# Kernel tuning notes

Measured on AMD Instinct MI355X. Metric: run time of the kernel, lower is better.

Reference implementation:

```python
import jax, jax.numpy as jnp
import numpy as np

NEG = -9.0e15


def setup_inputs() -> dict:
    key = jax.random.key(0)
    ks = jax.random.split(key, 8)
    N, D_IN, D_OUT, EMB = 100000, 128, 128, 64
    E, NPE = 50000, 32   # hyperedges, nodes per edge
    U, EPN = 50000, 32   # output nodes, edges per node
    stdv = 1.0 / np.sqrt(D_IN)
    return {
        "x": jax.random.normal(ks[0], (N, D_IN), dtype=jnp.float32),
        "seq": jax.random.randint(ks[1], (E, NPE), 0, N, dtype=jnp.int64),
        "text2emb": jax.random.normal(ks[2], (100, EMB), dtype=jnp.float32),
        "useq": jax.random.randint(ks[3], (U, EPN), 0, E, dtype=jnp.int64),
        "data_idx": jax.random.randint(ks[4], (U,), 0, U, dtype=jnp.int64),
        "weight1": jax.random.uniform(ks[5], (D_IN, D_OUT), jnp.float32, -stdv, stdv),
        "weight2": jax.random.uniform(ks[6], (D_OUT, D_OUT), jnp.float32, -stdv, stdv),
        "weight3": jax.random.uniform(ks[7], (100, EMB), jnp.float32, -stdv, stdv),
    }


def _masked_mean_weights(idx):
    # softmax over a {1, -9e15} mask -> uniform weights over nonzero slots
    logits = jnp.where(idx > 0, jnp.float32(1.0), jnp.float32(NEG))
    return jax.nn.softmax(logits, axis=1)


def reference(x, seq, text2emb, useq, data_idx, weight1, weight2, weight3):
    # text_weight is computed in the original forward but never used
    w3n = weight3 / jnp.linalg.norm(weight3, axis=1, keepdims=True)
    cos = w3n @ w3n.T
    _text_weight = cos.mean(axis=1).mean()  # scalar, unused downstream

    h = x @ weight1                              # [N, D_OUT]
    adj_fea = h[seq]                             # [E, NPE, D_OUT] gather
    w = _masked_mean_weights(seq)                # [E, NPE]
    edge = jnp.einsum("enc,en->ec", adj_fea, w)  # [E, D_OUT]
    # dropout is identity in eval mode
    edge = jax.nn.relu(edge)
    e1 = edge @ weight2                          # [E, D_OUT]

    edge_fea = e1[useq]                          # [U, EPN, D_OUT] gather
    uw = _masked_mean_weights(useq)              # [U, EPN]
    node = jnp.einsum("uec,ue->uc", edge_fea, uw)  # [U, D_OUT]
    return node
```

## Files before the change

kernel.cpp:

```cpp
#include <hip/hip_runtime.h>
#include <hip/hip_bf16.h>

#define N_NODES  100000
#define E_EDGES  50000
#define U_NODES  50000
#define D        128
#define NPE      32

typedef __attribute__((ext_vector_type(8))) short short8;
typedef __attribute__((ext_vector_type(4))) unsigned short u16x4;
typedef __attribute__((ext_vector_type(4))) float f32x4;

static __device__ __forceinline__ unsigned short f2bf_bits(float f) {
    unsigned u = __float_as_uint(f);
    return (unsigned short)((u + 0x7fffu + ((u >> 16) & 1u)) >> 16);
}

__global__ void prep_wt(const float* __restrict__ w1, const float* __restrict__ w2,
                        unsigned short* __restrict__ wt) {
    const int t = blockIdx.x * 256 + threadIdx.x;
    const int which = t >> 14;
    const int e = t & 16383;
    const int k = e >> 7, c = e & 127;
    const float* w = which ? w2 : w1;
    wt[which * 16384 + c * 128 + k] = f2bf_bits(w[e]);
}

__global__ __launch_bounds__(256) void convert_x(const float* __restrict__ x,
                                                 unsigned short* __restrict__ xb,
                                                 int n8) {
    const int i = blockIdx.x * 256 + threadIdx.x;
    if (i >= n8) return;
    const float4 a = ((const float4*)x)[2 * i];
    const float4 b = ((const float4*)x)[2 * i + 1];
    uint4 o;
    o.x = (unsigned)f2bf_bits(a.x) | ((unsigned)f2bf_bits(a.y) << 16);
    o.y = (unsigned)f2bf_bits(a.z) | ((unsigned)f2bf_bits(a.w) << 16);
    o.z = (unsigned)f2bf_bits(b.x) | ((unsigned)f2bf_bits(b.y) << 16);
    o.w = (unsigned)f2bf_bits(b.z) | ((unsigned)f2bf_bits(b.w) << 16);
    ((uint4*)xb)[i] = o;
}

template<int OUT_BF16, int RELU>
__global__ __launch_bounds__(256) void gather_mean4(
        const unsigned short* __restrict__ src, const int* __restrict__ idx,
        void* __restrict__ dst, int M) {
    const int wid = (int)((blockIdx.x * blockDim.x + threadIdx.x) >> 6);
    if (wid >= M) return;
    const int lane = threadIdx.x & 63;
    const int g = lane >> 4;
    const int c = lane & 15;

    int my = 0;
    if (lane < NPE) my = idx[(size_t)wid * NPE + lane];
    const unsigned long long b = __ballot(lane < NPE && my > 0);
    const int count = __popcll(b);
    const float scale = 1.0f / (float)(count > 0 ? count : NPE);
    const bool take_all = (count == 0);

    uint4 v[8];
    float w[8];
#pragma unroll
    for (int i = 0; i < 8; ++i) {
        const int id = __shfl(my, i * 4 + g);
        w[i] = (take_all || id > 0) ? scale : 0.0f;
        v[i] = *(const uint4*)(src + (size_t)id * D + c * 8);
    }
    asm volatile("" ::: "memory");

    float acc[8] = {0.f, 0.f, 0.f, 0.f, 0.f, 0.f, 0.f, 0.f};
#pragma unroll
    for (int i = 0; i < 8; ++i) {
        acc[0] = fmaf(__uint_as_float(v[i].x << 16),         w[i], acc[0]);
        acc[1] = fmaf(__uint_as_float(v[i].x & 0xffff0000u), w[i], acc[1]);
        acc[2] = fmaf(__uint_as_float(v[i].y << 16),         w[i], acc[2]);
        acc[3] = fmaf(__uint_as_float(v[i].y & 0xffff0000u), w[i], acc[3]);
        acc[4] = fmaf(__uint_as_float(v[i].z << 16),         w[i], acc[4]);
        acc[5] = fmaf(__uint_as_float(v[i].z & 0xffff0000u), w[i], acc[5]);
        acc[6] = fmaf(__uint_as_float(v[i].w << 16),         w[i], acc[6]);
        acc[7] = fmaf(__uint_as_float(v[i].w & 0xffff0000u), w[i], acc[7]);
    }

#pragma unroll
    for (int i = 0; i < 8; ++i) {
        acc[i] += __shfl_xor(acc[i], 16);
        acc[i] += __shfl_xor(acc[i], 32);
        if (RELU) acc[i] = fmaxf(acc[i], 0.f);
    }

    if (lane < 16) {
        if (OUT_BF16) {
            uint4 o;
            o.x = (unsigned)f2bf_bits(acc[0]) | ((unsigned)f2bf_bits(acc[1]) << 16);
            o.y = (unsigned)f2bf_bits(acc[2]) | ((unsigned)f2bf_bits(acc[3]) << 16);
            o.z = (unsigned)f2bf_bits(acc[4]) | ((unsigned)f2bf_bits(acc[5]) << 16);
            o.w = (unsigned)f2bf_bits(acc[6]) | ((unsigned)f2bf_bits(acc[7]) << 16);
            *(uint4*)((unsigned short*)dst + (size_t)wid * D + c * 8) = o;
        } else {
            float* dp = (float*)dst + (size_t)wid * D + c * 8;
            *(float4*)dp = make_float4(acc[0], acc[1], acc[2], acc[3]);
            *(float4*)(dp + 4) = make_float4(acc[4], acc[5], acc[6], acc[7]);
        }
    }
}

__global__ __launch_bounds__(256) void gemm12(const unsigned short* __restrict__ gx,
                                              const unsigned short* __restrict__ Wt,
                                              unsigned short* __restrict__ e1, int M) {
    __shared__ unsigned short sW1[128 * 136];
    __shared__ unsigned short sW2[128 * 136];
    __shared__ unsigned short sA[64 * 136];
    const int tid = threadIdx.x;

    {
        const float4* w4 = (const float4*)Wt;
#pragma unroll
        for (int j = 0; j < 8; ++j) {
            const int i = tid + j * 256;
            const int r = i >> 4, c16 = i & 15;
            *(float4*)&sW1[r * 136 + c16 * 8] = w4[i];
            *(float4*)&sW2[r * 136 + c16 * 8] = w4[2048 + i];
        }
    }

    const int ntiles = (M + 63) >> 6;
    const int lane = tid & 63;
    const int wv = tid >> 6;
    const int r16 = lane & 15;
    const int hi = lane >> 4;

    float4 pf[4];
    auto load_tile = [&](int tile) {
        const int row0 = tile << 6;
#pragma unroll
        for (int j = 0; j < 4; ++j) {
            const int i = tid + j * 256;
            int gr = row0 + (i >> 4); if (gr >= M) gr = M - 1;
            pf[j] = *(const float4*)&gx[(size_t)gr * D + (i & 15) * 8];
        }
    };

    int tile = blockIdx.x;
    if (tile >= ntiles) return;
    load_tile(tile);

    while (tile < ntiles) {
#pragma unroll
        for (int j = 0; j < 4; ++j) {
            const int i = tid + j * 256;
            *(float4*)&sA[(i >> 4) * 136 + (i & 15) * 8] = pf[j];
        }
        __syncthreads();

        const int next = tile + gridDim.x;
        if (next < ntiles) load_tile(next);
        asm volatile("" ::: "memory");

        short8 af[4];
#pragma unroll
        for (int kt = 0; kt < 4; ++kt)
            af[kt] = *(const short8*)&sA[(wv * 16 + r16) * 136 + kt * 32 + hi * 8];

        f32x4 acc[8];
#pragma unroll
        for (int ct = 0; ct < 8; ++ct) acc[ct] = (f32x4){0.f, 0.f, 0.f, 0.f};
#pragma unroll
        for (int ct = 0; ct < 8; ++ct)
#pragma unroll
            for (int kt = 0; kt < 4; ++kt) {
                const short8 bf = *(const short8*)&sW1[(ct * 16 + r16) * 136 + kt * 32 + hi * 8];
                acc[ct] = __builtin_amdgcn_mfma_f32_16x16x32_bf16(af[kt], bf, acc[ct], 0, 0, 0);
            }

#pragma unroll
        for (int ct = 0; ct < 8; ++ct)
#pragma unroll
            for (int i = 0; i < 4; ++i)
                sA[(wv * 16 + hi * 4 + i) * 136 + ct * 16 + r16] =
                    f2bf_bits(fmaxf(acc[ct][i], 0.f));

        short8 af2[4];
#pragma unroll
        for (int kt = 0; kt < 4; ++kt)
            af2[kt] = *(const short8*)&sA[(wv * 16 + r16) * 136 + kt * 32 + hi * 8];

        f32x4 acc2[8];
#pragma unroll
        for (int ct = 0; ct < 8; ++ct) acc2[ct] = (f32x4){0.f, 0.f, 0.f, 0.f};
#pragma unroll
        for (int ct = 0; ct < 8; ++ct)
#pragma unroll
            for (int kt = 0; kt < 4; ++kt) {
                const short8 bf = *(const short8*)&sW2[(ct * 16 + r16) * 136 + kt * 32 + hi * 8];
                acc2[ct] = __builtin_amdgcn_mfma_f32_16x16x32_bf16(af2[kt], bf, acc2[ct], 0, 0, 0);
            }

#pragma unroll
        for (int ct = 0; ct < 8; ++ct)
#pragma unroll
            for (int i = 0; i < 4; ++i)
                sA[(wv * 16 + hi * 4 + i) * 136 + ct * 16 + r16] = f2bf_bits(acc2[ct][i]);
        __syncthreads();

        const int row0 = tile << 6;
        const int nrows = min(64, M - row0);
#pragma unroll
        for (int j = 0; j < 4; ++j) {
            const int i = tid + j * 256;
            const int r = i >> 4, cc = i & 15;
            if (r < nrows)
                *(float4*)&e1[(size_t)(row0 + r) * D + cc * 8] =
                    *(const float4*)&sA[r * 136 + cc * 8];
        }
        __syncthreads();
        tile = next;
    }
}

extern "C" void kernel_launch(void* const* d_in, const int* in_sizes, int n_in,
                              void* d_out, int out_size, void* d_ws, size_t ws_size,
                              hipStream_t stream) {
    const float* x    = (const float*)d_in[0];
    const int*   seq  = (const int*)d_in[1];
    const int*   useq = (const int*)d_in[3];
    const float* w1   = (const float*)d_in[5];
    const float* w2   = (const float*)d_in[6];
    float* out = (float*)d_out;

    unsigned short* wt = (unsigned short*)d_ws;
    unsigned short* xb = wt + 2 * 16384;
    unsigned short* gx = xb + (size_t)N_NODES * D;
    unsigned short* e1 = gx + (size_t)E_EDGES * D;

    prep_wt<<<128, 256, 0, stream>>>(w1, w2, wt);
    convert_x<<<(N_NODES * D / 8 + 255) / 256, 256, 0, stream>>>(x, xb, N_NODES * D / 8);

    gather_mean4<1, 0><<<(E_EDGES * 64) / 256, 256, 0, stream>>>(xb, seq, gx, E_EDGES);

    gemm12<<<512, 256, 0, stream>>>(gx, wt, e1, E_EDGES);

    gather_mean4<0, 0><<<(U_NODES * 64) / 256, 256, 0, stream>>>(e1, useq, out, U_NODES);
}
```

Measured before the change: 232.6 us.

## Restructure fused GEMM into one-shot 1024-thread tiles with XOR-swizzled LDS, inline-asm gather loads

The persistent 64-row tile loop in the fused two-GEMM kernel is replaced by one 256-row tile per 1024-thread block, with no cross-tile prefetch. LDS padding is replaced by an XOR swizzle to avoid bank conflicts. The gather kernel now issues its row loads through inline global_load_dwordx4 asm followed by an explicit waitcnt, so all eight loads stay in flight together. The larger blocks use about 128KB of LDS, which limits residency to one block per CU and drops overlap of loads with compute.

```diff
diff --git a/kernel.cpp b/kernel.cpp
--- a/kernel.cpp
+++ b/kernel.cpp
@@ -10,10 +10,15 @@
 typedef __attribute__((ext_vector_type(8))) short short8;
 typedef __attribute__((ext_vector_type(4))) unsigned short u16x4;
 typedef __attribute__((ext_vector_type(4))) float f32x4;
+typedef __attribute__((ext_vector_type(4))) unsigned int u32x4;
 
 static __device__ __forceinline__ unsigned short f2bf_bits(float f) {
     unsigned u = __float_as_uint(f);
     return (unsigned short)((u + 0x7fffu + ((u >> 16) & 1u)) >> 16);
+}
+
+static __device__ __forceinline__ int swz(int row, int bytecol) {
+    return row * 256 + ((((bytecol >> 4) ^ (row & 7)) << 4) | (bytecol & 15));
 }
 
 __global__ void prep_wt(const float* __restrict__ w1, const float* __restrict__ w2,
@@ -58,15 +63,19 @@
     const float scale = 1.0f / (float)(count > 0 ? count : NPE);
     const bool take_all = (count == 0);
 
-    uint4 v[8];
+    const unsigned short* base = src + c * 8;
+    u32x4 v[8];
     float w[8];
 #pragma unroll
     for (int i = 0; i < 8; ++i) {
         const int id = __shfl(my, i * 4 + g);
         w[i] = (take_all || id > 0) ? scale : 0.0f;
-        v[i] = *(const uint4*)(src + (size_t)id * D + c * 8);
-    }
-    asm volatile("" ::: "memory");
+        const unsigned short* p = base + (size_t)id * D;
+        asm volatile("global_load_dwordx4 %0, %1, off"
+                     : "=v"(v[i]) : "v"(p));
+    }
+    asm volatile("s_waitcnt vmcnt(0)" ::: "memory");
+    __builtin_amdgcn_sched_barrier(0);
 
     float acc[8] = {0.f, 0.f, 0.f, 0.f, 0.f, 0.f, 0.f, 0.f};
 #pragma unroll
@@ -104,116 +113,98 @@
     }
 }
 
-__global__ __launch_bounds__(256) void gemm12(const unsigned short* __restrict__ gx,
-                                              const unsigned short* __restrict__ Wt,
-                                              unsigned short* __restrict__ e1, int M) {
-    __shared__ unsigned short sW1[128 * 136];
-    __shared__ unsigned short sW2[128 * 136];
-    __shared__ unsigned short sA[64 * 136];
+__global__ __launch_bounds__(1024) void gemm12(const unsigned short* __restrict__ gx,
+                                               const unsigned short* __restrict__ Wt,
+                                               unsigned short* __restrict__ e1, int M) {
+    __shared__ unsigned short sW1[128 * 128];
+    __shared__ unsigned short sW2[128 * 128];
+    __shared__ unsigned short sA[256 * 128];
     const int tid = threadIdx.x;
+    const int row0 = blockIdx.x * 256;
+    const int nrows = min(256, M - row0);
 
     {
         const float4* w4 = (const float4*)Wt;
 #pragma unroll
-        for (int j = 0; j < 8; ++j) {
-            const int i = tid + j * 256;
-            const int r = i >> 4, c16 = i & 15;
-            *(float4*)&sW1[r * 136 + c16 * 8] = w4[i];
-            *(float4*)&sW2[r * 136 + c16 * 8] = w4[2048 + i];
-        }
-    }
-
-    const int ntiles = (M + 63) >> 6;
+        for (int j = 0; j < 2; ++j) {
+            const int i = tid + j * 1024;
+            const int r = i >> 4, cc = (i & 15) * 16;
+            *(float4*)((char*)sW1 + swz(r, cc)) = w4[i];
+            *(float4*)((char*)sW2 + swz(r, cc)) = w4[2048 + i];
+        }
+    }
+    {
+#pragma unroll
+        for (int j = 0; j < 4; ++j) {
+            const int i = tid + j * 1024;
+            const int r = i >> 4, cc = (i & 15) * 16;
+            int gr = row0 + r; if (gr >= M) gr = M - 1;
+            *(float4*)((char*)sA + swz(r, cc)) =
+                *(const float4*)&gx[(size_t)gr * D + (i & 15) * 8];
+        }
+    }
+    __syncthreads();
+
     const int lane = tid & 63;
     const int wv = tid >> 6;
     const int r16 = lane & 15;
     const int hi = lane >> 4;
-
-    float4 pf[4];
-    auto load_tile = [&](int tile) {
-        const int row0 = tile << 6;
-#pragma unroll
-        for (int j = 0; j < 4; ++j) {
-            const int i = tid + j * 256;
-            int gr = row0 + (i >> 4); if (gr >= M) gr = M - 1;
-            pf[j] = *(const float4*)&gx[(size_t)gr * D + (i & 15) * 8];
-        }
-    };
-
-    int tile = blockIdx.x;
-    if (tile >= ntiles) return;
-    load_tile(tile);
-
-    while (tile < ntiles) {
-#pragma unroll
-        for (int j = 0; j < 4; ++j) {
-            const int i = tid + j * 256;
-            *(float4*)&sA[(i >> 4) * 136 + (i & 15) * 8] = pf[j];
-        }
-        __syncthreads();
-
-        const int next = tile + gridDim.x;
-        if (next < ntiles) load_tile(next);
-        asm volatile("" ::: "memory");
-
-        short8 af[4];
-#pragma unroll
-        for (int kt = 0; kt < 4; ++kt)
-            af[kt] = *(const short8*)&sA[(wv * 16 + r16) * 136 + kt * 32 + hi * 8];
-
-        f32x4 acc[8];
-#pragma unroll
-        for (int ct = 0; ct < 8; ++ct) acc[ct] = (f32x4){0.f, 0.f, 0.f, 0.f};
-#pragma unroll
-        for (int ct = 0; ct < 8; ++ct)
-#pragma unroll
-            for (int kt = 0; kt < 4; ++kt) {
-                const short8 bf = *(const short8*)&sW1[(ct * 16 + r16) * 136 + kt * 32 + hi * 8];
-                acc[ct] = __builtin_amdgcn_mfma_f32_16x16x32_bf16(af[kt], bf, acc[ct], 0, 0, 0);
-            }
-
-#pragma unroll
-        for (int ct = 0; ct < 8; ++ct)
-#pragma unroll
-            for (int i = 0; i < 4; ++i)
-                sA[(wv * 16 + hi * 4 + i) * 136 + ct * 16 + r16] =
-                    f2bf_bits(fmaxf(acc[ct][i], 0.f));
-
-        short8 af2[4];
-#pragma unroll
-        for (int kt = 0; kt < 4; ++kt)
-            af2[kt] = *(const short8*)&sA[(wv * 16 + r16) * 136 + kt * 32 + hi * 8];
-
-        f32x4 acc2[8];
-#pragma unroll
-        for (int ct = 0; ct < 8; ++ct) acc2[ct] = (f32x4){0.f, 0.f, 0.f, 0.f};
-#pragma unroll
-        for (int ct = 0; ct < 8; ++ct)
-#pragma unroll
-            for (int kt = 0; kt < 4; ++kt) {
-                const short8 bf = *(const short8*)&sW2[(ct * 16 + r16) * 136 + kt * 32 + hi * 8];
-                acc2[ct] = __builtin_amdgcn_mfma_f32_16x16x32_bf16(af2[kt], bf, acc2[ct], 0, 0, 0);
-            }
-
-#pragma unroll
-        for (int ct = 0; ct < 8; ++ct)
-#pragma unroll
-            for (int i = 0; i < 4; ++i)
-                sA[(wv * 16 + hi * 4 + i) * 136 + ct * 16 + r16] = f2bf_bits(acc2[ct][i]);
-        __syncthreads();
-
-        const int row0 = tile << 6;
-        const int nrows = min(64, M - row0);
-#pragma unroll
-        for (int j = 0; j < 4; ++j) {
-            const int i = tid + j * 256;
-            const int r = i >> 4, cc = i & 15;
-            if (r < nrows)
-                *(float4*)&e1[(size_t)(row0 + r) * D + cc * 8] =
-                    *(const float4*)&sA[r * 136 + cc * 8];
-        }
-        __syncthreads();
-        tile = next;
+    const int Ra = wv * 16 + r16;
+
+    short8 af[4];
+#pragma unroll
+    for (int kt = 0; kt < 4; ++kt)
+        af[kt] = *(const short8*)((char*)sA + swz(Ra, kt * 64 + hi * 16));
+
+    f32x4 acc[8];
+#pragma unroll
+    for (int ct = 0; ct < 8; ++ct) acc[ct] = (f32x4){0.f, 0.f, 0.f, 0.f};
+#pragma unroll
+    for (int ct = 0; ct < 8; ++ct)
+#pragma unroll
+        for (int kt = 0; kt < 4; ++kt) {
+            const short8 bf = *(const short8*)((char*)sW1 + swz(ct * 16 + r16, kt * 64 + hi * 16));
+            acc[ct] = __builtin_amdgcn_mfma_f32_16x16x32_bf16(af[kt], bf, acc[ct], 0, 0, 0);
+        }
+
+#pragma unroll
+    for (int ct = 0; ct < 8; ++ct)
+#pragma unroll
+        for (int i = 0; i < 4; ++i)
+            *(unsigned short*)((char*)sA + swz(wv * 16 + hi * 4 + i, (ct * 16 + r16) * 2)) =
+                f2bf_bits(fmaxf(acc[ct][i], 0.f));
+
+    short8 af2[4];
+#pragma unroll
+    for (int kt = 0; kt < 4; ++kt)
+        af2[kt] = *(const short8*)((char*)sA + swz(Ra, kt * 64 + hi * 16));
+
+    f32x4 acc2[8];
+#pragma unroll
+    for (int ct = 0; ct < 8; ++ct) acc2[ct] = (f32x4){0.f, 0.f, 0.f, 0.f};
+#pragma unroll
+    for (int ct = 0; ct < 8; ++ct)
+#pragma unroll
+        for (int kt = 0; kt < 4; ++kt) {
+            const short8 bf = *(const short8*)((char*)sW2 + swz(ct * 16 + r16, kt * 64 + hi * 16));
+            acc2[ct] = __builtin_amdgcn_mfma_f32_16x16x32_bf16(af2[kt], bf, acc2[ct], 0, 0, 0);
+        }
+
+#pragma unroll
+    for (int ct = 0; ct < 8; ++ct)
+#pragma unroll
+        for (int i = 0; i < 4; ++i)
+            *(unsigned short*)((char*)sA + swz(wv * 16 + hi * 4 + i, (ct * 16 + r16) * 2)) =
+                f2bf_bits(acc2[ct][i]);
+    __syncthreads();
+
+#pragma unroll
+    for (int j = 0; j < 4; ++j) {
+        const int i = tid + j * 1024;
+        const int r = i >> 4, cc = i & 15;
+        if (r < nrows)
+            *(float4*)&e1[(size_t)(row0 + r) * D + cc * 8] =
+                *(const float4*)((char*)sA + swz(r, cc * 16));
     }
 }
 
@@ -237,7 +228,7 @@
 
     gather_mean4<1, 0><<<(E_EDGES * 64) / 256, 256, 0, stream>>>(xb, seq, gx, E_EDGES);
 
-    gemm12<<<512, 256, 0, stream>>>(gx, wt, e1, E_EDGES);
+    gemm12<<<(E_EDGES + 255) / 256, 1024, 0, stream>>>(gx, wt, e1, E_EDGES);
 
     gather_mean4<0, 0><<<(U_NODES * 64) / 256, 256, 0, stream>>>(e1, useq, out, U_NODES);
 }
```

New measurement: 216.9 us. -6.7%, faster.
